# Optimization experiments

Measured on AMD Instinct MI355X. Metric: run time of the kernel, lower is better.

## Reference

```python
import jax, jax.numpy as jnp
import numpy as np

IN_F = 256
OUT_F = 256
ALPHA = 0.2  # leakyrelu negative slope


def setup_inputs() -> dict:
    key = jax.random.key(0)
    k1, k2, k3 = jax.random.split(key, 3)
    B, N = 64, 1024
    x_loc = jax.random.normal(k1, (B, N, IN_F), dtype=jnp.float32)
    # xavier_uniform with gain=1.414
    def xavier(k, shape, gain=1.414):
        fan_in, fan_out = shape[0], shape[1]
        bound = gain * np.sqrt(6.0 / (fan_in + fan_out))
        return jax.random.uniform(k, shape, jnp.float32, -bound, bound)
    W = xavier(k2, (IN_F, OUT_F))
    a = xavier(k3, (2 * OUT_F, 1))
    return {"x_loc": x_loc, "W": W, "a": a, "entity_num": N}


def reference(x_loc, W, a, entity_num):
    # h: [B, N, F]
    h = jnp.matmul(x_loc, W)
    F_out = W.shape[1]
    a1 = a[:F_out, 0]   # [F]
    a2 = a[F_out:, 0]   # [F]
    # score(i, j) = leakyrelu(a1 . h_i + a2 . h_j)  -- decomposition of
    # matmul(cat(h_i, h_j), a); identical math, avoids O(N^2 * 2F) tensor.
    s1 = jnp.einsum('bnf,f->bn', h, a1)  # [B, N]
    s2 = jnp.einsum('bnf,f->bn', h, a2)  # [B, N]
    e = s1[:, :, None] + s2[:, None, :]  # [B, N, N]
    e = jnp.where(e > 0, e, ALPHA * e)   # leakyrelu(alpha=0.2)
    attention = jax.nn.softmax(e, axis=2)
    h_prime = jnp.matmul(attention, h)   # [B, N, F]
    return h_prime  # concat=False -> no elu
```

## Files before the change

kernel.cpp:

```cpp
#include <hip/hip_runtime.h>


typedef unsigned short u16;
typedef unsigned int   u32;
typedef unsigned long long u64;
typedef float  f32x4  __attribute__((ext_vector_type(4)));
typedef __bf16 bf16x8 __attribute__((ext_vector_type(8)));
typedef __bf16 bf16x4 __attribute__((ext_vector_type(4)));

#define NB    64
#define NENT  1024
#define FD    256
#define NROWS (NB * NENT)
#define ALPHA 0.2f

typedef __attribute__((address_space(1))) const void* gas_ptr;
typedef __attribute__((address_space(3))) void*       las_ptr;
__device__ __forceinline__ void gload16(const void* g, void* l) {
  __builtin_amdgcn_global_load_lds((gas_ptr)g, (las_ptr)l, 16, 0, 0);
}

__global__ __launch_bounds__(256) void k_wa(const float* __restrict__ W,
                                            const float* __restrict__ a,
                                            float* __restrict__ Wa1,
                                            float* __restrict__ Wa2) {
  const int k = blockIdx.x, f = threadIdx.x;
  const float w = W[(size_t)k * FD + f];
  float p1 = w * a[f];
  float p2 = w * a[FD + f];
#pragma unroll
  for (int off = 1; off < 64; off <<= 1) {
    p1 += __shfl_xor(p1, off, 64);
    p2 += __shfl_xor(p2, off, 64);
  }
  __shared__ float r1[4], r2[4];
  const int wv = f >> 6, lane = f & 63;
  if (lane == 0) { r1[wv] = p1; r2[wv] = p2; }
  __syncthreads();
  if (f == 0) {
    Wa1[k] = r1[0] + r1[1] + r1[2] + r1[3];
    Wa2[k] = r2[0] + r2[1] + r2[2] + r2[3];
  }
}

__global__ __launch_bounds__(256) void k_wt(const float* __restrict__ W,
                                            u16* __restrict__ Wt) {
  __shared__ float tile[64][65];
  const int t = threadIdx.x;
  const int ki = blockIdx.x >> 2, fi = blockIdx.x & 3;
  const int k0 = ki * 64, f0 = fi * 64;
  const int r = t >> 4, c4 = (t & 15) * 4;
#pragma unroll
  for (int it = 0; it < 4; ++it) {
    const int row = r + it * 16;
    float4 v = *(const float4*)&W[(size_t)(k0 + row) * FD + f0 + c4];
    tile[row][c4 + 0] = v.x; tile[row][c4 + 1] = v.y;
    tile[row][c4 + 2] = v.z; tile[row][c4 + 3] = v.w;
  }
  __syncthreads();
#pragma unroll
  for (int it = 0; it < 4; ++it) {
    const int fr = r + it * 16;
    bf16x4 pk;
    pk[0] = (__bf16)tile[c4 + 0][fr]; pk[1] = (__bf16)tile[c4 + 1][fr];
    pk[2] = (__bf16)tile[c4 + 2][fr]; pk[3] = (__bf16)tile[c4 + 3][fr];
    *(bf16x4*)&Wt[(size_t)(f0 + fr) * FD + k0 + c4] = pk;
  }
}

__global__ __launch_bounds__(512, 2) void k_h(
    const float* __restrict__ x, const u16* __restrict__ Wt,
    const float* __restrict__ Wa1g, const float* __restrict__ Wa2g,
    u16* __restrict__ h, float* __restrict__ s1, float* __restrict__ s2) {
  __shared__ __align__(16) char smem[67584];
  u16* Ab = (u16*)smem;
  u16* Bb = (u16*)(smem + 32768);
  float* wa1 = (float*)(smem + 65536);
  float* wa2 = wa1 + FD;
  const int t = threadIdx.x;
  const int lane = t & 63, wv = t >> 6;
  const int wr = wv >> 2, wc = wv & 3;
  const int g16 = lane >> 4, c15 = lane & 15;
  const int p = blockIdx.x;
  const int lb = (p & 7) * 32 + (p >> 3);
  const int rT = lb * 256;
  if (t < FD) { wa1[t] = Wa1g[t]; wa2[t] = Wa2g[t]; }
  const int row = t >> 1, half = t & 1;
  const float* xsrc = x + (size_t)(rT + row) * FD + half * 16;
  float p1 = 0.f, p2 = 0.f;
  f32x4 acc[8][4];
  const f32x4 vz = {0.f, 0.f, 0.f, 0.f};
#pragma unroll
  for (int i = 0; i < 8; ++i)
#pragma unroll
    for (int j = 0; j < 4; ++j) acc[i][j] = vz;

  auto stage = [&](int nb, int kc, const float4& f0, const float4& f1,
                   const float4& f2, const float4& f3) {
    const int k0n = kc * 32;
    const int d0 = t;
    gload16(Wt + (size_t)(d0 & 255) * FD + k0n + (d0 >> 8) * 8,
            (char*)Bb + nb * 8192 * 2 + d0 * 16);
    const int d1 = t + 512;
    gload16(Wt + (size_t)(d1 & 255) * FD + k0n + (d1 >> 8) * 8,
            (char*)Bb + nb * 8192 * 2 + d1 * 16);
    bf16x8 w0, w1;
    w0[0] = (__bf16)f0.x; w0[1] = (__bf16)f0.y;
    w0[2] = (__bf16)f0.z; w0[3] = (__bf16)f0.w;
    w0[4] = (__bf16)f1.x; w0[5] = (__bf16)f1.y;
    w0[6] = (__bf16)f1.z; w0[7] = (__bf16)f1.w;
    w1[0] = (__bf16)f2.x; w1[1] = (__bf16)f2.y;
    w1[2] = (__bf16)f2.z; w1[3] = (__bf16)f2.w;
    w1[4] = (__bf16)f3.x; w1[5] = (__bf16)f3.y;
    w1[6] = (__bf16)f3.z; w1[7] = (__bf16)f3.w;
    *(bf16x8*)(Ab + ((nb * 4 + half * 2) * 256 + row) * 8) = w0;
    *(bf16x8*)(Ab + ((nb * 4 + half * 2 + 1) * 256 + row) * 8) = w1;
    const int kb = k0n + half * 16;
    p1 += f0.x*wa1[kb+ 0] + f0.y*wa1[kb+ 1] + f0.z*wa1[kb+ 2] + f0.w*wa1[kb+ 3]
        + f1.x*wa1[kb+ 4] + f1.y*wa1[kb+ 5] + f1.z*wa1[kb+ 6] + f1.w*wa1[kb+ 7]
        + f2.x*wa1[kb+ 8] + f2.y*wa1[kb+ 9] + f2.z*wa1[kb+10] + f2.w*wa1[kb+11]
        + f3.x*wa1[kb+12] + f3.y*wa1[kb+13] + f3.z*wa1[kb+14] + f3.w*wa1[kb+15];
    p2 += f0.x*wa2[kb+ 0] + f0.y*wa2[kb+ 1] + f0.z*wa2[kb+ 2] + f0.w*wa2[kb+ 3]
        + f1.x*wa2[kb+ 4] + f1.y*wa2[kb+ 5] + f1.z*wa2[kb+ 6] + f1.w*wa2[kb+ 7]
        + f2.x*wa2[kb+ 8] + f2.y*wa2[kb+ 9] + f2.z*wa2[kb+10] + f2.w*wa2[kb+11]
        + f3.x*wa2[kb+12] + f3.y*wa2[kb+13] + f3.z*wa2[kb+14] + f3.w*wa2[kb+15];
  };
  auto mfma_step = [&](int cb) {
    bf16x8 bfv[4];
#pragma unroll
    for (int fj = 0; fj < 4; ++fj)
      bfv[fj] = *(const bf16x8*)(Bb + ((cb * 4 + g16) * 256 + wc * 64 + fj * 16 + c15) * 8);
#pragma unroll
    for (int fi = 0; fi < 8; ++fi) {
      bf16x8 af = *(const bf16x8*)(Ab + ((cb * 4 + g16) * 256 + wr * 128 + fi * 16 + c15) * 8);
#pragma unroll
      for (int fj = 0; fj < 4; ++fj)
        acc[fi][fj] = __builtin_amdgcn_mfma_f32_16x16x32_bf16(
            af, bfv[fj], acc[fi][fj], 0, 0, 0);
    }
  };

  float4 xc0 = *(const float4*)(xsrc +  0);
  float4 xc1 = *(const float4*)(xsrc +  4);
  float4 xc2 = *(const float4*)(xsrc +  8);
  float4 xc3 = *(const float4*)(xsrc + 12);
  float4 xb0 = *(const float4*)(xsrc + 32);
  float4 xb1 = *(const float4*)(xsrc + 36);
  float4 xb2 = *(const float4*)(xsrc + 40);
  float4 xb3 = *(const float4*)(xsrc + 44);
  float4 xa0 = *(const float4*)(xsrc + 64);
  float4 xa1 = *(const float4*)(xsrc + 68);
  float4 xa2 = *(const float4*)(xsrc + 72);
  float4 xa3 = *(const float4*)(xsrc + 76);
  __syncthreads();
  stage(0, 0, xc0, xc1, xc2, xc3);
  __syncthreads();
#pragma unroll 1
  for (int ks2 = 0; ks2 < 4; ++ks2) {
    stage(1, 2 * ks2 + 1, xb0, xb1, xb2, xb3);
    if (2 * ks2 + 3 < 8) {
      const float* s = xsrc + (2 * ks2 + 3) * 32;
      xb0 = *(const float4*)(s);      xb1 = *(const float4*)(s + 4);
      xb2 = *(const float4*)(s + 8);  xb3 = *(const float4*)(s + 12);
    }
    mfma_step(0);
    __syncthreads();
    if (2 * ks2 + 2 < 8) {
      stage(0, 2 * ks2 + 2, xa0, xa1, xa2, xa3);
      if (2 * ks2 + 4 < 8) {
        const float* s = xsrc + (2 * ks2 + 4) * 32;
        xa0 = *(const float4*)(s);      xa1 = *(const float4*)(s + 4);
        xa2 = *(const float4*)(s + 8);  xa3 = *(const float4*)(s + 12);
      }
    }
    mfma_step(1);
    __syncthreads();
  }
  p1 += __shfl_xor(p1, 1, 64);
  p2 += __shfl_xor(p2, 1, 64);
  if (half == 0) { s1[rT + row] = p1; s2[rT + row] = p2; }
  u16* ep = (u16*)smem;
#pragma unroll
  for (int hh = 0; hh < 4; ++hh) {
    if (wr == (hh >> 1)) {
#pragma unroll
      for (int fi2 = 0; fi2 < 4; ++fi2) {
        const int erow = fi2 * 16 + 4 * g16;
#pragma unroll
        for (int fj = 0; fj < 4; ++fj) {
          const int col = wc * 64 + fj * 16 + c15;
#pragma unroll
          for (int r = 0; r < 4; ++r) {
            __bf16 bv = (__bf16)acc[(hh & 1) * 4 + fi2][fj][r];
            ep[(erow + r) * 264 + col] = __builtin_bit_cast(u16, bv);
          }
        }
      }
    }
    __syncthreads();
    const int rrow = t >> 3, seg = t & 7;
    const u16* src = ep + rrow * 264 + seg * 32;
    u16* dst = h + (size_t)(rT + hh * 64 + rrow) * FD + seg * 32;
#pragma unroll
    for (int q = 0; q < 4; ++q)
      *(uint4*)(dst + q * 8) = *(const uint4*)(src + q * 8);
    __syncthreads();
  }
}

__global__ __launch_bounds__(512) void k_sc(
    const u16* __restrict__ h, const float* __restrict__ s1,
    const float* __restrict__ s2, float* __restrict__ out) {
  __shared__ __align__(16) u64  kp[1024];
  __shared__ __align__(16) float key[1024];
  __shared__ __align__(16) u16   pid[1024];
  __shared__ __align__(16) float e2l[1024], e2al[1024];
  __shared__ __align__(16) float Su[1032], Sv[1032];
  __shared__ __align__(16) float c1l[1024], c2l[1024];
  __shared__ __align__(16) u32   cnt[1025];
  __shared__ __align__(16) u16   ibl[1032];
  __shared__ __align__(16) u16   iol[1024];
  __shared__ float UpS[8];
  __shared__ float Up[8][64], Vp[8][64];
  const int t = threadIdx.x;
  const int b = blockIdx.y, fc = blockIdx.x;
  const int w = t >> 6, lane = t & 63;

  auto packkey = [&](int j) {
    float v = s2[(size_t)b * NENT + j];
    u32 u = __builtin_bit_cast(u32, v);
    u32 su = u ^ (u32)(((int)u >> 31) | 0x80000000);
    kp[j] = ((u64)su << 32) | (u32)j;
  };
  packkey(t); packkey(t + 512);
  __syncthreads();
#pragma unroll 1
  for (int kk = 2; kk <= 1024; kk <<= 1) {
#pragma unroll 1
    for (int j = kk >> 1; j > 0; j >>= 1) {
      if (j >= 64) __syncthreads();
      else asm volatile("" ::: "memory");
      const int i  = ((t & ~(j - 1)) << 1) | (t & (j - 1));
      const int ix = i | j;
      const bool up = ((i & kk) == 0);
      u64 a = kp[i], c = kp[ix];
      const bool sw = up ? (a > c) : (a < c);
      if (sw) { kp[i] = c; kp[ix] = a; }
    }
  }
  __syncthreads();
  auto unpack = [&](int r) {
    u64 v = kp[r];
    u32 su = (u32)(v >> 32);
    u32 ub = (su & 0x80000000u) ? (su ^ 0x80000000u) : ~su;
    float kv = __builtin_bit_cast(float, ub);
    key[r] = kv;
    pid[r] = (u16)(v & 0xFFFFu);
    e2l[r] = __expf(kv);
    e2al[r] = __expf(ALPHA * kv);
  };
  unpack(t); unpack(t + 512);
  __syncthreads();
  auto scanx = [&](const float* src, float* dst) {
    float a = src[2 * t], bb = src[2 * t + 1];
    float s = a + bb;
    float inc = s;
#pragma unroll
    for (int d = 1; d < 64; d <<= 1) {
      float o = __shfl_up(inc, d, 64);
      if (lane >= d) inc += o;
    }
    if (lane == 63) UpS[w] = inc;
    __syncthreads();
    float woff = 0.f;
#pragma unroll
    for (int w2 = 0; w2 < 8; ++w2) { float pv = UpS[w2]; if (w2 < w) woff += pv; }
    float P = woff + inc - s;
    dst[2 * t] = P; dst[2 * t + 1] = P + a;
    if (t == 511) dst[1024] = P + s;
    __syncthreads();
  };
  scanx(e2l, Su);
  scanx(e2al, Sv);
  const float s2max = key[1023];
  const float SuN = Su[1024];
  int kfA, kfB;
  cnt[t] = 0; cnt[t + 512] = 0;
  if (t == 0) cnt[1024] = 0;
  __syncthreads();
#pragma unroll
  for (int hi = 0; hi < 2; ++hi) {
    const int i = t + hi * 512;
    const float s1v = s1[(size_t)b * NENT + i];
    const float th = -s1v;
    int kf = 0;
#pragma unroll
    for (int d = 1024; d >= 1; d >>= 1)
      if (kf + d <= 1024 && key[kf + d - 1] < th) kf += d;
    const float qm = s1v + s2max;
    const float m = fmaxf(qm, ALPHA * qm);
    const float en1 = __expf(fminf(s1v - m, 80.f));
    const float en2 = __expf(fminf(ALPHA * s1v - m, 80.f));
    const float Z = en1 * (SuN - Su[kf]) + en2 * Sv[kf];
    const float rZ = 1.f / Z;
    c1l[i] = en1 * rZ; c2l[i] = en2 * rZ;
    if (hi == 0) kfA = kf; else kfB = kf;
    atomicAdd(&cnt[kf], 1u);
  }
  __syncthreads();
  {
    float a = (float)cnt[2 * t], bb = (float)cnt[2 * t + 1];
    cnt[2 * t] = 0; cnt[2 * t + 1] = 0;
    if (t == 0) cnt[1024] = 0;
    float s = a + bb;
    float inc = s;
#pragma unroll
    for (int d = 1; d < 64; d <<= 1) {
      float o = __shfl_up(inc, d, 64);
      if (lane >= d) inc += o;
    }
    if (lane == 63) UpS[w] = inc;
    __syncthreads();
    float woff = 0.f;
#pragma unroll
    for (int w2 = 0; w2 < 8; ++w2) { float pv = UpS[w2]; if (w2 < w) woff += pv; }
    float P = woff + inc - s;
    ibl[2 * t] = (u16)P; ibl[2 * t + 1] = (u16)(P + a);
    if (t == 511) ibl[1024] = (u16)(P + s);
  }
  __syncthreads();
  {
    int pos = (int)ibl[kfA] + (int)atomicAdd(&cnt[kfA], 1u);
    pos = pos < 1023 ? pos : 1023;
    iol[pos] = (u16)t;
    int posB = (int)ibl[kfB] + (int)atomicAdd(&cnt[kfB], 1u);
    posB = posB < 1023 ? posB : 1023;
    iol[posB] = (u16)(t + 512);
  }
  __syncthreads();
  const int col = fc * 64 + lane;
  const u16* hb = h + (size_t)b * NENT * FD + col;
  const int r0 = w * 128;
  float ha[8], hc[8];
  auto ldh8 = [&](float* dv, int rb) {
    uint4 praw = *(const uint4*)&pid[rb];
    const u16* pp = (const u16*)&praw;
#pragma unroll
    for (int u2 = 0; u2 < 8; ++u2) {
      u32 raw = hb[(size_t)pp[u2] * FD];
      dv[u2] = __builtin_bit_cast(float, raw << 16);
    }
  };
  auto lde8 = [&](float* E, float* A2, int rb) {
    *(float4*)&E[0]  = *(const float4*)&e2l[rb];
    *(float4*)&E[4]  = *(const float4*)&e2l[rb + 4];
    *(float4*)&A2[0] = *(const float4*)&e2al[rb];
    *(float4*)&A2[4] = *(const float4*)&e2al[rb + 4];
  };
  float U = 0.f, V = 0.f;
  ldh8(ha, r0);
#pragma unroll 1
  for (int g = 0; g < 8; ++g) {
    const int rb = r0 + g * 16;
    ldh8(hc, rb + 8);
    float E[8], A2[8];
    lde8(E, A2, rb);
#pragma unroll
    for (int u2 = 0; u2 < 8; ++u2) { U += E[u2] * ha[u2]; V += A2[u2] * ha[u2]; }
    if (g < 7) ldh8(ha, rb + 16);
    lde8(E, A2, rb + 8);
#pragma unroll
    for (int u2 = 0; u2 < 8; ++u2) { U += E[u2] * hc[u2]; V += A2[u2] * hc[u2]; }
  }
  Up[w][lane] = U; Vp[w][lane] = V;
  __syncthreads();
  float Uoff = 0.f, Voff = 0.f, UN = 0.f, VN = 0.f;
#pragma unroll
  for (int w2 = 0; w2 < 8; ++w2) {
    float a = Up[w2][lane], c = Vp[w2][lane];
    if (w2 < w) { Uoff += a; Voff += c; }
    UN += a; VN += c;
  }
  U = Uoff; V = Voff;
  ldh8(ha, r0);
#pragma unroll 1
  for (int g = 0; g < 8; ++g) {
    const int rb = r0 + g * 16;
    ldh8(hc, rb + 8);
    float E[8], A2[8];
    lde8(E, A2, rb);
    uint4 ibraw = *(const uint4*)&ibl[rb];
    const u16* ib = (const u16*)&ibraw;
    u16 ibn = ibl[rb + 8];
#pragma unroll
    for (int u2 = 0; u2 < 8; ++u2) {
      const int e0 = ib[u2], e1 = (u2 < 7) ? ib[u2 + 1] : (int)ibn;
      for (int idx = e0; idx < e1; ++idx) {
        const int i = iol[idx];
        out[((size_t)b * NENT + i) * FD + col] = c1l[i] * (UN - U) + c2l[i] * V;
      }
      U += E[u2] * ha[u2]; V += A2[u2] * ha[u2];
    }
    if (g < 7) ldh8(ha, rb + 16);
    lde8(E, A2, rb + 8);
    uint4 ibraw2 = *(const uint4*)&ibl[rb + 8];
    const u16* ib2 = (const u16*)&ibraw2;
    u16 ibn2 = ibl[rb + 16];
#pragma unroll
    for (int u2 = 0; u2 < 8; ++u2) {
      const int e0 = ib2[u2], e1 = (u2 < 7) ? ib2[u2 + 1] : (int)ibn2;
      for (int idx = e0; idx < e1; ++idx) {
        const int i = iol[idx];
        out[((size_t)b * NENT + i) * FD + col] = c1l[i] * (UN - U) + c2l[i] * V;
      }
      U += E[u2] * hc[u2]; V += A2[u2] * hc[u2];
    }
  }
  if (w == 7) {
    const int e0 = ibl[1024];
    for (int idx = e0; idx < 1024; ++idx) {
      const int i = iol[idx];
      out[((size_t)b * NENT + i) * FD + col] = c1l[i] * (UN - U) + c2l[i] * V;
    }
  }
}

extern "C" void kernel_launch(void* const* d_in, const int* in_sizes, int n_in,
                              void* d_out, int out_size, void* d_ws, size_t ws_size,
                              hipStream_t stream) {
  const float* x = (const float*)d_in[0];
  const float* W = (const float*)d_in[1];
  const float* a = (const float*)d_in[2];
  float* out = (float*)d_out;

  char* ws = (char*)d_ws;
  u16*   h   = (u16*)ws;
  float* s1  = (float*)(ws + (size_t)33554432);
  float* s2  = s1 + NROWS;
  float* Wa1 = s2 + NROWS;
  float* Wa2 = Wa1 + FD;
  u16*   Wt  = (u16*)(Wa2 + FD);

  k_wa<<<dim3(256), dim3(256), 0, stream>>>(W, a, Wa1, Wa2);
  k_wt<<<dim3(16), dim3(256), 0, stream>>>(W, Wt);
  k_h<<<dim3(256), dim3(512), 0, stream>>>(x, Wt, Wa1, Wa2, h, s1, s2);
  k_sc<<<dim3(4, NB), dim3(512), 0, stream>>>(h, s1, s2, out);
}
```

Measured before the change: 93.44 us.

## Split sort from emit and pre-transpose sorted h into column-major layout

The fused score kernel is split into three kernels. The first sorts keys and computes the per-row coefficients once per batch instead of once per column block. The second gathers h rows in sorted order and transposes them so each column is contiguous. The emit kernel then reads h with contiguous 16-byte loads instead of scattered 2-byte gathers, which removes the fourfold redundant sorting and the uncoalesced gathers. The cost is two extra launches and an extra round trip of a 32 MB transposed copy plus the scratch arrays through global memory.

```diff
diff --git a/kernel.cpp b/kernel.cpp
--- a/kernel.cpp
+++ b/kernel.cpp
@@ -208,9 +208,11 @@
   }
 }
 
-__global__ __launch_bounds__(512) void k_sc(
-    const u16* __restrict__ h, const float* __restrict__ s1,
-    const float* __restrict__ s2, float* __restrict__ out) {
+__global__ __launch_bounds__(512) void k_srt(
+    const float* __restrict__ s1, const float* __restrict__ s2,
+    float* __restrict__ e2D, float* __restrict__ e2aD,
+    float* __restrict__ c1D, float* __restrict__ c2D,
+    u16* __restrict__ pidD, u16* __restrict__ iolD, u16* __restrict__ iblD) {
   __shared__ __align__(16) u64  kp[1024];
   __shared__ __align__(16) float key[1024];
   __shared__ __align__(16) u16   pid[1024];
@@ -221,9 +223,8 @@
   __shared__ __align__(16) u16   ibl[1032];
   __shared__ __align__(16) u16   iol[1024];
   __shared__ float UpS[8];
-  __shared__ float Up[8][64], Vp[8][64];
   const int t = threadIdx.x;
-  const int b = blockIdx.y, fc = blockIdx.x;
+  const int b = blockIdx.x;
   const int w = t >> 6, lane = t & 63;
 
   auto packkey = [&](int j) {
@@ -338,39 +339,95 @@
     iol[posB] = (u16)(t + 512);
   }
   __syncthreads();
-  const int col = fc * 64 + lane;
-  const u16* hb = h + (size_t)b * NENT * FD + col;
+  const size_t ob = (size_t)b * NENT;
+  e2D [ob + t] = e2l[t];  e2D [ob + t + 512] = e2l[t + 512];
+  e2aD[ob + t] = e2al[t]; e2aD[ob + t + 512] = e2al[t + 512];
+  c1D [ob + t] = c1l[t];  c1D [ob + t + 512] = c1l[t + 512];
+  c2D [ob + t] = c2l[t];  c2D [ob + t + 512] = c2l[t + 512];
+  *(u32*)&pidD[ob + 2 * t] = *(const u32*)&pid[2 * t];
+  *(u32*)&iolD[ob + 2 * t] = *(const u32*)&iol[2 * t];
+  *(u32*)&iblD[(size_t)b * 1040 + 2 * t] = *(const u32*)&ibl[2 * t];
+  if (t == 0) iblD[(size_t)b * 1040 + 1024] = ibl[1024];
+}
+
+__global__ __launch_bounds__(512) void k_tr(
+    const u16* __restrict__ h, const u16* __restrict__ pidD,
+    u16* __restrict__ hsT) {
+  __shared__ u16 pidl[1024];
+  __shared__ u16 tile[2][64][72];
+  const int t = threadIdx.x;
+  const int cg = blockIdx.x, b = blockIdx.y;
+  const int c0 = cg * 64;
+  *(u32*)&pidl[2 * t] = *(const u32*)&pidD[(size_t)b * NENT + 2 * t];
+  const int rs = t >> 3, seg = t & 7;
+  const u16* hb = h + (size_t)b * NENT * FD;
+  u16* hTb = hsT + (size_t)b * FD * NENT;
+  __syncthreads();
+  {
+    const int srow = pidl[rs];
+    *(uint4*)&tile[0][rs][seg * 8] =
+        *(const uint4*)&hb[(size_t)srow * FD + c0 + seg * 8];
+  }
+  __syncthreads();
+#pragma unroll 1
+  for (int it = 0; it < 16; ++it) {
+    if (it < 15) {
+      const int srow = pidl[(it + 1) * 64 + rs];
+      *(uint4*)&tile[(it + 1) & 1][rs][seg * 8] =
+          *(const uint4*)&hb[(size_t)srow * FD + c0 + seg * 8];
+    }
+    const int cs = t >> 3, rseg = t & 7;
+    u16 tmp[8];
+#pragma unroll
+    for (int q = 0; q < 8; ++q) tmp[q] = tile[it & 1][rseg * 8 + q][cs];
+    *(uint4*)&hTb[(size_t)(c0 + cs) * NENT + it * 64 + rseg * 8] =
+        *(const uint4*)tmp;
+    __syncthreads();
+  }
+}
+
+__global__ __launch_bounds__(512) void k_emit(
+    const u16* __restrict__ hsT, const float* __restrict__ e2D,
+    const float* __restrict__ e2aD, const float* __restrict__ c1D,
+    const float* __restrict__ c2D, const u16* __restrict__ iolD,
+    const u16* __restrict__ iblD, float* __restrict__ out) {
+  __shared__ __align__(16) float e2l[1024], e2al[1024];
+  __shared__ __align__(16) float c1l[1024], c2l[1024];
+  __shared__ __align__(16) u16 ibl[1032], iol[1024];
+  __shared__ float Up[8][64], Vp[8][64];
+  const int t = threadIdx.x;
+  const int cg = blockIdx.x, b = blockIdx.y;
+  const int w = t >> 6, lane = t & 63;
+  const size_t ob = (size_t)b * NENT;
+  *(float2*)&e2l[2 * t]  = *(const float2*)&e2D[ob + 2 * t];
+  *(float2*)&e2al[2 * t] = *(const float2*)&e2aD[ob + 2 * t];
+  *(float2*)&c1l[2 * t]  = *(const float2*)&c1D[ob + 2 * t];
+  *(float2*)&c2l[2 * t]  = *(const float2*)&c2D[ob + 2 * t];
+  *(u32*)&iol[2 * t] = *(const u32*)&iolD[ob + 2 * t];
+  *(u32*)&ibl[2 * t] = *(const u32*)&iblD[(size_t)b * 1040 + 2 * t];
+  if (t == 0) ibl[1024] = iblD[(size_t)b * 1040 + 1024];
+  __syncthreads();
+  const int col = cg * 64 + lane;
+  const u16* hcol = hsT + ((size_t)b * FD + col) * NENT;
   const int r0 = w * 128;
-  float ha[8], hc[8];
-  auto ldh8 = [&](float* dv, int rb) {
-    uint4 praw = *(const uint4*)&pid[rb];
-    const u16* pp = (const u16*)&praw;
-#pragma unroll
-    for (int u2 = 0; u2 < 8; ++u2) {
-      u32 raw = hb[(size_t)pp[u2] * FD];
-      dv[u2] = __builtin_bit_cast(float, raw << 16);
-    }
-  };
-  auto lde8 = [&](float* E, float* A2, int rb) {
-    *(float4*)&E[0]  = *(const float4*)&e2l[rb];
-    *(float4*)&E[4]  = *(const float4*)&e2l[rb + 4];
-    *(float4*)&A2[0] = *(const float4*)&e2al[rb];
-    *(float4*)&A2[4] = *(const float4*)&e2al[rb + 4];
+  auto qf = [&](u32 uu, float* lo, float* hi) {
+    *lo = __builtin_bit_cast(float, uu << 16);
+    *hi = __builtin_bit_cast(float, uu & 0xFFFF0000u);
   };
   float U = 0.f, V = 0.f;
-  ldh8(ha, r0);
 #pragma unroll 1
-  for (int g = 0; g < 8; ++g) {
-    const int rb = r0 + g * 16;
-    ldh8(hc, rb + 8);
-    float E[8], A2[8];
-    lde8(E, A2, rb);
-#pragma unroll
-    for (int u2 = 0; u2 < 8; ++u2) { U += E[u2] * ha[u2]; V += A2[u2] * ha[u2]; }
-    if (g < 7) ldh8(ha, rb + 16);
-    lde8(E, A2, rb + 8);
-#pragma unroll
-    for (int u2 = 0; u2 < 8; ++u2) { U += E[u2] * hc[u2]; V += A2[u2] * hc[u2]; }
+  for (int g = 0; g < 16; ++g) {
+    const int rb = r0 + g * 8;
+    uint4 raw = *(const uint4*)(hcol + rb);
+    float4 E0 = *(const float4*)&e2l[rb], E1 = *(const float4*)&e2l[rb + 4];
+    float4 A0 = *(const float4*)&e2al[rb], A1 = *(const float4*)&e2al[rb + 4];
+    float f0, f1, f2, f3, f4, f5, f6, f7;
+    qf(raw.x, &f0, &f1); qf(raw.y, &f2, &f3);
+    qf(raw.z, &f4, &f5); qf(raw.w, &f6, &f7);
+    U += E0.x * f0 + E0.y * f1 + E0.z * f2 + E0.w * f3
+       + E1.x * f4 + E1.y * f5 + E1.z * f6 + E1.w * f7;
+    V += A0.x * f0 + A0.y * f1 + A0.z * f2 + A0.w * f3
+       + A1.x * f4 + A1.y * f5 + A1.z * f6 + A1.w * f7;
   }
   Up[w][lane] = U; Vp[w][lane] = V;
   __syncthreads();
@@ -382,38 +439,30 @@
     UN += a; VN += c;
   }
   U = Uoff; V = Voff;
-  ldh8(ha, r0);
 #pragma unroll 1
-  for (int g = 0; g < 8; ++g) {
-    const int rb = r0 + g * 16;
-    ldh8(hc, rb + 8);
-    float E[8], A2[8];
-    lde8(E, A2, rb);
+  for (int g = 0; g < 16; ++g) {
+    const int rb = r0 + g * 8;
+    uint4 raw = *(const uint4*)(hcol + rb);
+    float4 E0 = *(const float4*)&e2l[rb], E1 = *(const float4*)&e2l[rb + 4];
+    float4 A0 = *(const float4*)&e2al[rb], A1 = *(const float4*)&e2al[rb + 4];
     uint4 ibraw = *(const uint4*)&ibl[rb];
     const u16* ib = (const u16*)&ibraw;
-    u16 ibn = ibl[rb + 8];
+    const int ibn = ibl[rb + 8];
+    float hf[8];
+    qf(raw.x, &hf[0], &hf[1]); qf(raw.y, &hf[2], &hf[3]);
+    qf(raw.z, &hf[4], &hf[5]); qf(raw.w, &hf[6], &hf[7]);
+    const float* Ep = (const float*)&E0;
+    float Ev[8] = {E0.x, E0.y, E0.z, E0.w, E1.x, E1.y, E1.z, E1.w};
+    float Av[8] = {A0.x, A0.y, A0.z, A0.w, A1.x, A1.y, A1.z, A1.w};
+    (void)Ep;
 #pragma unroll
     for (int u2 = 0; u2 < 8; ++u2) {
-      const int e0 = ib[u2], e1 = (u2 < 7) ? ib[u2 + 1] : (int)ibn;
+      const int e0 = ib[u2], e1 = (u2 < 7) ? (int)ib[u2 + 1] : ibn;
       for (int idx = e0; idx < e1; ++idx) {
         const int i = iol[idx];
         out[((size_t)b * NENT + i) * FD + col] = c1l[i] * (UN - U) + c2l[i] * V;
       }
-      U += E[u2] * ha[u2]; V += A2[u2] * ha[u2];
-    }
-    if (g < 7) ldh8(ha, rb + 16);
-    lde8(E, A2, rb + 8);
-    uint4 ibraw2 = *(const uint4*)&ibl[rb + 8];
-    const u16* ib2 = (const u16*)&ibraw2;
-    u16 ibn2 = ibl[rb + 16];
-#pragma unroll
-    for (int u2 = 0; u2 < 8; ++u2) {
-      const int e0 = ib2[u2], e1 = (u2 < 7) ? ib2[u2 + 1] : (int)ibn2;
-      for (int idx = e0; idx < e1; ++idx) {
-        const int i = iol[idx];
-        out[((size_t)b * NENT + i) * FD + col] = c1l[i] * (UN - U) + c2l[i] * V;
-      }
-      U += E[u2] * hc[u2]; V += A2[u2] * hc[u2];
+      U += Ev[u2] * hf[u2]; V += Av[u2] * hf[u2];
     }
   }
   if (w == 7) {
@@ -434,15 +483,27 @@
   float* out = (float*)d_out;
 
   char* ws = (char*)d_ws;
-  u16*   h   = (u16*)ws;
-  float* s1  = (float*)(ws + (size_t)33554432);
-  float* s2  = s1 + NROWS;
-  float* Wa1 = s2 + NROWS;
-  float* Wa2 = Wa1 + FD;
-  u16*   Wt  = (u16*)(Wa2 + FD);
+  u16*   h    = (u16*)ws;
+  u16*   hsT  = (u16*)(ws + (size_t)33554432);
+  float* s1   = (float*)(ws + (size_t)67108864);
+  float* s2   = s1 + NROWS;
+  float* Wa1  = s2 + NROWS;
+  float* Wa2  = Wa1 + FD;
+  u16*   Wt   = (u16*)(Wa2 + FD);
+  float* e2D  = (float*)((char*)Wt + 131072);
+  float* e2aD = e2D + NROWS;
+  float* c1D  = e2aD + NROWS;
+  float* c2D  = c1D + NROWS;
+  u16*   pidD = (u16*)(c2D + NROWS);
+  u16*   iolD = pidD + NROWS;
+  u16*   iblD = iolD + NROWS;
 
   k_wa<<<dim3(256), dim3(256), 0, stream>>>(W, a, Wa1, Wa2);
   k_wt<<<dim3(16), dim3(256), 0, stream>>>(W, Wt);
   k_h<<<dim3(256), dim3(512), 0, stream>>>(x, Wt, Wa1, Wa2, h, s1, s2);
-  k_sc<<<dim3(4, NB), dim3(512), 0, stream>>>(h, s1, s2, out);
-}
+  k_srt<<<dim3(NB), dim3(512), 0, stream>>>(s1, s2, e2D, e2aD, c1D, c2D,
+                                            pidD, iolD, iblD);
+  k_tr<<<dim3(4, NB), dim3(512), 0, stream>>>(h, pidD, hsT);
+  k_emit<<<dim3(4, NB), dim3(512), 0, stream>>>(hsT, e2D, e2aD, c1D, c2D,
+                                                iolD, iblD, out);
+}
```

Measured after the change: 116.6 us. 24.8% more time.
